# Kernel optimization log

Hardware: AMD Instinct MI355X
Metric: run time of the kernel (lower is better)

Reference implementation:

```python
import jax, jax.numpy as jnp
import numpy as np

N = 100000
E = 1600000
D_IN = 128
HID = 128
LN_EPS = 1e-5
GIN_EPS = 0.0  # PyG GINConv default eps


def setup_inputs() -> dict:
    key = jax.random.key(0)
    ks = jax.random.split(key, 8)
    x = jax.random.normal(ks[0], (N, D_IN), dtype=jnp.float32)
    edge_index = jax.random.randint(ks[1], (2, E), 0, N, dtype=jnp.int64)
    s1 = 1.0 / np.sqrt(D_IN)
    s2 = 1.0 / np.sqrt(HID)
    W1 = jax.random.uniform(ks[2], (D_IN, HID), jnp.float32, -s1, s1)
    b1 = jnp.zeros((HID,), jnp.float32)
    W2 = jax.random.uniform(ks[3], (HID, HID), jnp.float32, -s2, s2)
    b2 = jnp.zeros((HID,), jnp.float32)
    gamma = jnp.ones((HID,), jnp.float32)
    beta = jnp.zeros((HID,), jnp.float32)
    Wres = jax.random.uniform(ks[4], (D_IN, HID), jnp.float32, -s1, s1)
    bres = jnp.zeros((HID,), jnp.float32)
    return {"x": x, "edge_index": edge_index, "W1": W1, "b1": b1,
            "W2": W2, "b2": b2, "gamma": gamma, "beta": beta,
            "Wres": Wres, "bres": bres}


def reference(x, edge_index, W1, b1, W2, b2, gamma, beta, Wres, bres):
    src, dst = edge_index[0], edge_index[1]
    # GIN sum aggregation: scatter-add source features onto targets. [N, D_IN]
    agg = jax.ops.segment_sum(x[src], dst, num_segments=N)
    h = (1.0 + GIN_EPS) * x + agg
    # GIN MLP: Linear -> ReLU -> Linear
    h = jax.nn.relu(h @ W1 + b1) @ W2 + b2
    # LayerNorm over hidden dim
    mu = jnp.mean(h, axis=-1, keepdims=True)
    var = jnp.mean(jnp.square(h - mu), axis=-1, keepdims=True)
    h = (h - mu) * jax.lax.rsqrt(var + LN_EPS) * gamma + beta
    # dropout p=0 is identity; residual linear path
    return h + (x @ Wres + bres)
```

## Files before the change

### kernel.cpp

```cpp
#include <hip/hip_runtime.h>

#define NN 100000
#define NE 1600000
#define D 128
#define RT 64
#define NB 196
#define CAP 9216
#define PADB 136
#define PB 12503
#define BUCKB 391

typedef unsigned short u16;
typedef __attribute__((ext_vector_type(8))) short bf16x8;
typedef __attribute__((ext_vector_type(4))) float f32x4;

__device__ __forceinline__ u16 f2bf(float f) {
  unsigned int u = __float_as_uint(f);
  u += 0x7fffu + ((u >> 16) & 1u);
  return (u16)(u >> 16);
}

__global__ __launch_bounds__(256) void prep_bucket_kernel(
    const float* __restrict__ x, const int* __restrict__ ei,
    const float* __restrict__ W1, const float* __restrict__ W2,
    const float* __restrict__ Wres,
    u16* __restrict__ xh, u16* __restrict__ wt,
    int* __restrict__ tail, unsigned* __restrict__ buf) {
  __shared__ int lhist[NB], lbase[NB];
  int b = blockIdx.x;
  int t = threadIdx.x;
  if (b < 12500) {
    int q = b * 256 + t;
    float4 v = ((const float4*)x)[q];
    uint2 pk;
    pk.x = (unsigned)f2bf(v.x) | ((unsigned)f2bf(v.y) << 16);
    pk.y = (unsigned)f2bf(v.z) | ((unsigned)f2bf(v.w) << 16);
    ((uint2*)xh)[q] = pk;
  } else if (b < PB) {
    const float* W = (b == 12500) ? Wres : (b == 12501) ? W1 : W2;
    u16* dst = wt + (size_t)(b - 12500) * 16384;
    for (int i = t; i < 16384; i += 256) {
      int n = i >> 7, k = i & 127;
      dst[i] = f2bf(W[k * 128 + n]);
    }
  } else {
    size_t e0 = (size_t)(b - PB) * 4096;
    int s[16], d[16];
    for (int j = t; j < NB; j += 256) lhist[j] = 0;
    __syncthreads();
#pragma unroll
    for (int k = 0; k < 16; ++k) {
      size_t e = e0 + t + (size_t)k * 256;
      if (e < NE) {
        d[k] = ei[NE + e];
        s[k] = ei[e];
        atomicAdd(&lhist[d[k] >> 9], 1);
      } else {
        d[k] = -1;
      }
    }
    __syncthreads();
    for (int j = t; j < NB; j += 256) {
      int c = lhist[j];
      lbase[j] = c ? atomicAdd(&tail[j], c) : 0;
      lhist[j] = 0;
    }
    __syncthreads();
#pragma unroll
    for (int k = 0; k < 16; ++k) {
      if (d[k] >= 0) {
        int bk = d[k] >> 9;
        int r = lbase[bk] + atomicAdd(&lhist[bk], 1);
        if (r < CAP)
          buf[(size_t)bk * CAP + r] = (unsigned)s[k] | ((unsigned)(d[k] & 511) << 17);
      }
    }
  }
}

__global__ __launch_bounds__(512) void build_csr(const unsigned* __restrict__ buf,
                                                 const int* __restrict__ tail,
                                                 int* __restrict__ cnt,
                                                 int* __restrict__ start,
                                                 int* __restrict__ csr) {
  __shared__ int lhist[512], lpre[512], lsum[64];
  int b = blockIdx.x, t = threadIdx.x;
  int nE = tail[b];
  if (nE > CAP) nE = CAP;
  size_t bBase = (size_t)b * CAP;
  lhist[t] = 0;
  __syncthreads();
  for (int i = t; i < nE; i += 512)
    atomicAdd(&lhist[buf[bBase + i] >> 17], 1);
  __syncthreads();
  if (t < 64) {
    int s = 0;
#pragma unroll
    for (int k = 0; k < 8; ++k) { int v = lhist[t * 8 + k]; lpre[t * 8 + k] = s; s += v; }
    lsum[t] = s;
  }
  __syncthreads();
  if (t == 0) {
    int s = 0;
    for (int k = 0; k < 64; ++k) { int v = lsum[k]; lsum[k] = s; s += v; }
  }
  __syncthreads();
  if (t < 64) {
    int o = lsum[t];
#pragma unroll
    for (int k = 0; k < 8; ++k) lpre[t * 8 + k] += o;
  }
  __syncthreads();
  int node = (b << 9) + t;
  if (node < NN) {
    cnt[node] = lhist[t];
    start[node] = (int)bBase + lpre[t];
  }
  lhist[t] = 0;
  __syncthreads();
  for (int i = t; i < nE; i += 512) {
    unsigned e = buf[bBase + i];
    int dl = e >> 17;
    int r = atomicAdd(&lhist[dl], 1);
    csr[bBase + lpre[dl] + r] = (int)(e & 0x1FFFFu);
  }
}

#define BFACC8(aL, aH, v)                                  \
  { aL.x += __uint_as_float((v).x << 16);                  \
    aL.y += __uint_as_float((v).x & 0xffff0000u);          \
    aL.z += __uint_as_float((v).y << 16);                  \
    aL.w += __uint_as_float((v).y & 0xffff0000u);          \
    aH.x += __uint_as_float((v).z << 16);                  \
    aH.y += __uint_as_float((v).z & 0xffff0000u);          \
    aH.z += __uint_as_float((v).w << 16);                  \
    aH.w += __uint_as_float((v).w & 0xffff0000u); }

__global__ __launch_bounds__(256, 6) void gather_kernel(const float* __restrict__ x,
                                                        const u16* __restrict__ xh,
                                                        const int* __restrict__ cnt,
                                                        const int* __restrict__ start,
                                                        const int* __restrict__ csr,
                                                        u16* __restrict__ h0h) {
  int g = blockIdx.x * 16 + (threadIdx.x >> 4);
  if (g >= NN) return;
  int lane = threadIdx.x & 15;
  int fo = lane * 8;
  int n = cnt[g];
  const int* sp = csr + start[g];

  float4 aL0 = make_float4(0.f, 0.f, 0.f, 0.f);
  float4 aH0 = aL0, aL1 = aL0, aH1 = aL0;

  int nfull = n & ~3;
  if (nfull > 0) {
    int s0 = sp[0], s1 = sp[1], s2 = sp[2], s3 = sp[3];
    uint4 v0 = *(const uint4*)&xh[(size_t)s0 * D + fo];
    uint4 v1 = *(const uint4*)&xh[(size_t)s1 * D + fo];
    uint4 v2 = *(const uint4*)&xh[(size_t)s2 * D + fo];
    uint4 v3 = *(const uint4*)&xh[(size_t)s3 * D + fo];
#pragma unroll 2
    for (int j = 4; j < nfull; j += 4) {
      int t0 = sp[j], t1 = sp[j + 1], t2 = sp[j + 2], t3 = sp[j + 3];
      uint4 w0 = *(const uint4*)&xh[(size_t)t0 * D + fo];
      uint4 w1 = *(const uint4*)&xh[(size_t)t1 * D + fo];
      uint4 w2 = *(const uint4*)&xh[(size_t)t2 * D + fo];
      uint4 w3 = *(const uint4*)&xh[(size_t)t3 * D + fo];
      BFACC8(aL0, aH0, v0); BFACC8(aL1, aH1, v1);
      BFACC8(aL0, aH0, v2); BFACC8(aL1, aH1, v3);
      v0 = w0; v1 = w1; v2 = w2; v3 = w3;
    }
    BFACC8(aL0, aH0, v0); BFACC8(aL1, aH1, v1);
    BFACC8(aL0, aH0, v2); BFACC8(aL1, aH1, v3);
  }
  for (int j = nfull; j < n; ++j) {
    uint4 v0 = *(const uint4*)&xh[(size_t)sp[j] * D + fo];
    BFACC8(aL0, aH0, v0);
  }

  const float* xp = &x[(size_t)g * D + fo];
  float4 x0 = *(const float4*)xp;
  float4 x1 = *(const float4*)(xp + 4);
  float h0 = x0.x + aL0.x + aL1.x;
  float h1 = x0.y + aL0.y + aL1.y;
  float h2 = x0.z + aL0.z + aL1.z;
  float h3 = x0.w + aL0.w + aL1.w;
  float h4 = x1.x + aH0.x + aH1.x;
  float h5 = x1.y + aH0.y + aH1.y;
  float h6 = x1.z + aH0.z + aH1.z;
  float h7 = x1.w + aH0.w + aH1.w;
  uint4 pk;
  pk.x = (unsigned)f2bf(h0) | ((unsigned)f2bf(h1) << 16);
  pk.y = (unsigned)f2bf(h2) | ((unsigned)f2bf(h3) << 16);
  pk.z = (unsigned)f2bf(h4) | ((unsigned)f2bf(h5) << 16);
  pk.w = (unsigned)f2bf(h6) | ((unsigned)f2bf(h7) << 16);
  *(uint4*)&h0h[(size_t)g * 256 + fo] = pk;
}

__global__ __launch_bounds__(256, 4) void fused_kernel(
    const u16* __restrict__ xh, const u16* __restrict__ h0h,
    const u16* __restrict__ wt,
    const float* __restrict__ b1, const float* __restrict__ b2,
    const float* __restrict__ gamma, const float* __restrict__ beta,
    const float* __restrict__ bres, float* __restrict__ out) {
  __shared__ u16 Hs[RT * PADB];

  const int t = threadIdx.x;
  const int w = t >> 6;
  const int lane = t & 63;
  const int quad = lane >> 4;
  const int l16 = lane & 15;
  const int row0 = blockIdx.x * RT;

#pragma unroll
  for (int i = 0; i < 8; ++i) {
    int v = t + i * 256;
    int r = v >> 5;
    int c4 = (v & 31) << 2;
    int row = row0 + r;
    uint2 val = make_uint2(0u, 0u);
    if (row < NN) val = *(const uint2*)&h0h[(size_t)row * 256 + c4];
    *(uint2*)&Hs[r * PADB + c4] = val;
  }

  f32x4 acc[8], accR[8];
  f32x4 zz = {0.f, 0.f, 0.f, 0.f};
#pragma unroll
  for (int i = 0; i < 8; ++i) { acc[i] = zz; accR[i] = zz; }

  auto gemmL = [&](const u16* __restrict__ W, f32x4 (&dd)[8]) {
    bf16x8 af[4];
#pragma unroll
    for (int s = 0; s < 4; ++s)
      af[s] = *(const bf16x8*)&Hs[(w * 16 + l16) * PADB + s * 32 + quad * 8];
#pragma unroll
    for (int nt = 0; nt < 8; ++nt) {
      const u16* wp = W + (size_t)(nt * 16 + l16) * D + quad * 8;
#pragma unroll
      for (int s = 0; s < 4; ++s) {
        bf16x8 bf = *(const bf16x8*)&wp[s * 32];
        dd[nt] = __builtin_amdgcn_mfma_f32_16x16x32_bf16(af[s], bf, dd[nt], 0, 0, 0);
      }
    }
  };

  {
    bf16x8 af[4];
#pragma unroll
    for (int s = 0; s < 4; ++s)
      af[s] = *(const bf16x8*)&xh[(size_t)(row0 + w * 16 + l16) * D + s * 32 + quad * 8];
#pragma unroll
    for (int nt = 0; nt < 8; ++nt) {
      const u16* wp = wt + (size_t)(nt * 16 + l16) * D + quad * 8;
#pragma unroll
      for (int s = 0; s < 4; ++s) {
        bf16x8 bf = *(const bf16x8*)&wp[s * 32];
        accR[nt] = __builtin_amdgcn_mfma_f32_16x16x32_bf16(af[s], bf, accR[nt], 0, 0, 0);
      }
    }
  }

  __syncthreads();
  gemmL(wt + 16384, acc);
  __syncthreads();

#pragma unroll
  for (int nt = 0; nt < 8; ++nt) {
    int col = nt * 16 + l16;
    float bb = b1[col];
#pragma unroll
    for (int r = 0; r < 4; ++r) {
      float hv = acc[nt][r] + bb;
      hv = hv > 0.f ? hv : 0.f;
      Hs[(w * 16 + quad * 4 + r) * PADB + col] = f2bf(hv);
      acc[nt][r] = 0.f;
    }
  }
  __syncthreads();
  gemmL(wt + 32768, acc);

  float b2v[8], gv[8], bev[8], brv[8];
#pragma unroll
  for (int nt = 0; nt < 8; ++nt) {
    int col = nt * 16 + l16;
    b2v[nt] = b2[col];
    gv[nt] = gamma[col];
    bev[nt] = beta[col];
    brv[nt] = bres[col];
  }
#pragma unroll
  for (int r = 0; r < 4; ++r) {
    float s = 0.f, s2 = 0.f;
#pragma unroll
    for (int nt = 0; nt < 8; ++nt) {
      float h = acc[nt][r] + b2v[nt];
      s += h;
      s2 += h * h;
    }
    for (int m = 1; m <= 8; m <<= 1) {
      s += __shfl_xor(s, m);
      s2 += __shfl_xor(s2, m);
    }
    float mu = s * 0.0078125f;
    float var = s2 * 0.0078125f - mu * mu;
    float rs = rsqrtf(var + 1e-5f);
    int row = row0 + w * 16 + quad * 4 + r;
    if (row < NN) {
#pragma unroll
      for (int nt = 0; nt < 8; ++nt) {
        float h = acc[nt][r] + b2v[nt];
        out[(size_t)row * D + nt * 16 + l16] =
            (h - mu) * rs * gv[nt] + bev[nt] + accR[nt][r] + brv[nt];
      }
    }
  }
}

extern "C" void kernel_launch(void* const* d_in, const int* in_sizes, int n_in,
                              void* d_out, int out_size, void* d_ws, size_t ws_size,
                              hipStream_t stream) {
  const float* x     = (const float*)d_in[0];
  const int*   ei    = (const int*)d_in[1];
  const float* W1    = (const float*)d_in[2];
  const float* b1    = (const float*)d_in[3];
  const float* W2    = (const float*)d_in[4];
  const float* b2    = (const float*)d_in[5];
  const float* gamma = (const float*)d_in[6];
  const float* beta  = (const float*)d_in[7];
  const float* Wres  = (const float*)d_in[8];
  const float* bres  = (const float*)d_in[9];
  float* out = (float*)d_out;

  int*      tail  = (int*)d_ws;
  unsigned* buf   = (unsigned*)(tail + 256);
  int*      cnt   = (int*)(buf + (size_t)NB * CAP);
  int*      start = cnt + NN;
  int*      csr   = start + NN;
  u16*      xh    = (u16*)(csr + (size_t)NB * CAP);
  u16*      wt    = xh + (size_t)NN * D;

  u16* h0h = (u16*)out;

  hipMemsetAsync(tail, 0, 256 * sizeof(int), stream);
  prep_bucket_kernel<<<PB + BUCKB, 256, 0, stream>>>(x, ei, W1, W2, Wres,
                                                     xh, wt, tail, buf);
  build_csr<<<NB, 512, 0, stream>>>(buf, tail, cnt, start, csr);
  gather_kernel<<<(NN + 15) / 16, 256, 0, stream>>>(x, xh, cnt, start, csr, h0h);
  fused_kernel<<<(NN + RT - 1) / RT, 256, 0, stream>>>(
      xh, h0h, wt, b1, b2, gamma, beta, bres, out);
}
```

Baseline: 317.7 us.

## Stage weight matrices in shared memory and read GEMM A operands directly from global

Each of the three weight matrices is copied into a padded LDS buffer before its GEMM, so B fragments are read from LDS instead of from global/L2 by every wave. The first-layer A operand is now loaded straight from global h0h rather than staged through LDS. This adds about 34KB of LDS per block and lowers the occupancy hint from 4 to 3 blocks, plus extra barriers between stages.

```diff
diff --git a/kernel.cpp b/kernel.cpp
--- a/kernel.cpp
+++ b/kernel.cpp
@@ -197,12 +197,13 @@
   *(uint4*)&h0h[(size_t)g * 256 + fo] = pk;
 }
 
-__global__ __launch_bounds__(256, 4) void fused_kernel(
+__global__ __launch_bounds__(256, 3) void fused_kernel(
     const u16* __restrict__ xh, const u16* __restrict__ h0h,
     const u16* __restrict__ wt,
     const float* __restrict__ b1, const float* __restrict__ b2,
     const float* __restrict__ gamma, const float* __restrict__ beta,
     const float* __restrict__ bres, float* __restrict__ out) {
+  __shared__ u16 Ws[128 * PADB];
   __shared__ u16 Hs[RT * PADB];
 
   const int t = threadIdx.x;
@@ -212,30 +213,31 @@
   const int l16 = lane & 15;
   const int row0 = blockIdx.x * RT;
 
-#pragma unroll
-  for (int i = 0; i < 8; ++i) {
-    int v = t + i * 256;
-    int r = v >> 5;
-    int c4 = (v & 31) << 2;
-    int row = row0 + r;
-    uint2 val = make_uint2(0u, 0u);
-    if (row < NN) val = *(const uint2*)&h0h[(size_t)row * 256 + c4];
-    *(uint2*)&Hs[r * PADB + c4] = val;
-  }
+  auto stageW = [&](const u16* __restrict__ src) {
+#pragma unroll
+    for (int i = 0; i < 16; ++i) {
+      int v = t + i * 256;
+      int r = v >> 5;
+      int c4 = (v & 31) << 2;
+      *(uint2*)&Ws[r * PADB + c4] = *(const uint2*)&src[r * D + c4];
+    }
+  };
 
   f32x4 acc[8], accR[8];
   f32x4 zz = {0.f, 0.f, 0.f, 0.f};
 #pragma unroll
   for (int i = 0; i < 8; ++i) { acc[i] = zz; accR[i] = zz; }
 
-  auto gemmL = [&](const u16* __restrict__ W, f32x4 (&dd)[8]) {
+  auto gemmGA = [&](const u16* __restrict__ Ag, int astride, f32x4 (&dd)[8]) {
     bf16x8 af[4];
+    int ar = row0 + w * 16 + l16;
+    if (ar > NN - 1) ar = NN - 1;
 #pragma unroll
     for (int s = 0; s < 4; ++s)
-      af[s] = *(const bf16x8*)&Hs[(w * 16 + l16) * PADB + s * 32 + quad * 8];
+      af[s] = *(const bf16x8*)&Ag[(size_t)ar * astride + s * 32 + quad * 8];
 #pragma unroll
     for (int nt = 0; nt < 8; ++nt) {
-      const u16* wp = W + (size_t)(nt * 16 + l16) * D + quad * 8;
+      const u16* wp = &Ws[(nt * 16 + l16) * PADB + quad * 8];
 #pragma unroll
       for (int s = 0; s < 4; ++s) {
         bf16x8 bf = *(const bf16x8*)&wp[s * 32];
@@ -243,25 +245,29 @@
       }
     }
   };
-
-  {
+  auto gemmLA = [&](f32x4 (&dd)[8]) {
     bf16x8 af[4];
 #pragma unroll
     for (int s = 0; s < 4; ++s)
-      af[s] = *(const bf16x8*)&xh[(size_t)(row0 + w * 16 + l16) * D + s * 32 + quad * 8];
+      af[s] = *(const bf16x8*)&Hs[(w * 16 + l16) * PADB + s * 32 + quad * 8];
 #pragma unroll
     for (int nt = 0; nt < 8; ++nt) {
-      const u16* wp = wt + (size_t)(nt * 16 + l16) * D + quad * 8;
+      const u16* wp = &Ws[(nt * 16 + l16) * PADB + quad * 8];
 #pragma unroll
       for (int s = 0; s < 4; ++s) {
         bf16x8 bf = *(const bf16x8*)&wp[s * 32];
-        accR[nt] = __builtin_amdgcn_mfma_f32_16x16x32_bf16(af[s], bf, accR[nt], 0, 0, 0);
-      }
-    }
-  }
-
-  __syncthreads();
-  gemmL(wt + 16384, acc);
+        dd[nt] = __builtin_amdgcn_mfma_f32_16x16x32_bf16(af[s], bf, dd[nt], 0, 0, 0);
+      }
+    }
+  };
+
+  stageW(wt);
+  __syncthreads();
+  gemmGA(xh, D, accR);
+  __syncthreads();
+  stageW(wt + 16384);
+  __syncthreads();
+  gemmGA(h0h, 256, acc);
   __syncthreads();
 
 #pragma unroll
@@ -276,8 +282,9 @@
       acc[nt][r] = 0.f;
     }
   }
-  __syncthreads();
-  gemmL(wt + 32768, acc);
+  stageW(wt + 32768);
+  __syncthreads();
+  gemmLA(acc);
 
   float b2v[8], gv[8], bev[8], brv[8];
 #pragma unroll
```

Measured after the change: 256.0 us. -19.4%, faster.
